# Kernel optimization log

Measured on AMD Instinct MI355X. Metric: run time of the kernel, lower is better.

## Reference

```python
import jax, jax.numpy as jnp
import numpy as np

N_COARSE = 100_000
M_FINE = 4 * N_COARSE
GRID = 128
C_IN, C_HID, C_OUT = 32, 64, 32
K3 = 27   # 3x3x3 neighborhood
K2 = 8    # 2x2x2 transposed-conv offsets


def setup_inputs() -> dict:
    rng = np.random.default_rng(0)
    # --- sparse coarse grid: N unique voxels in GRID^3 ---
    lin = np.sort(rng.choice(GRID ** 3, size=N_COARSE, replace=False))
    cx, cy, cz = lin // (GRID * GRID), (lin // GRID) % GRID, lin % GRID
    coords = np.stack([cx, cy, cz], 1).astype(np.int64)
    # --- rulebook: neighbor index per voxel per 3^3 offset (sentinel = N) ---
    offs = np.array([(dx, dy, dz) for dx in (-1, 0, 1) for dy in (-1, 0, 1) for dz in (-1, 0, 1)])
    nbr = np.full((N_COARSE, K3), N_COARSE, np.int32)
    for k in range(K3):
        nc = coords + offs[k]
        valid = ((nc >= 0) & (nc < GRID)).all(1)
        nlin = nc[:, 0] * GRID * GRID + nc[:, 1] * GRID + nc[:, 2]
        pos = np.clip(np.searchsorted(lin, nlin), 0, N_COARSE - 1)
        found = valid & (lin[pos] == nlin)
        nbr[found, k] = pos[found].astype(np.int32)
    # --- fine grid: 4 distinct children (of 8) per coarse voxel ---
    child = np.argsort(rng.random((N_COARSE, K2)), axis=1)[:, :4].astype(np.int32)
    parent_idx = np.repeat(np.arange(N_COARSE, dtype=np.int32), 4)
    offset_idx = child.reshape(-1)

    key = jax.random.key(0)
    ks = jax.random.split(key, 16)
    nrm = lambda k, sh, fan: (jax.random.normal(k, sh, jnp.float32) / np.sqrt(fan)).astype(jnp.float32)
    return {
        "feats_in": jax.random.normal(ks[0], (N_COARSE, C_IN), jnp.float32),
        "x_up_feats": jax.random.normal(ks[1], (M_FINE, C_OUT), jnp.float32),
        "nbr_idx": jnp.asarray(nbr),
        "parent_idx": jnp.asarray(parent_idx),
        "offset_idx": jnp.asarray(offset_idx),
        "W_enc1": nrm(ks[2], (K3, C_IN, C_HID), K3 * C_IN),
        "b_enc1": jnp.zeros((C_HID,), jnp.float32),
        "W_enc2": nrm(ks[3], (K3, C_HID, C_HID), K3 * C_HID),
        "b_enc2": jnp.zeros((C_HID,), jnp.float32),
        "W_enc3": nrm(ks[4], (K3, C_HID, C_HID), K3 * C_HID),
        "b_enc3": jnp.zeros((C_HID,), jnp.float32),
        "W_t": nrm(ks[5], (K2, C_HID, C_HID), C_HID),
        "b_t": jnp.zeros((C_HID,), jnp.float32),
        "W_d1": nrm(ks[6], (C_HID, C_HID), C_HID),
        "b_d1": jnp.zeros((C_HID,), jnp.float32),
        "W_d2": nrm(ks[7], (C_HID, C_OUT), C_HID),
        "b_d2": jnp.zeros((C_OUT,), jnp.float32),
    }


def _sparse_conv3(x, nbr, W, b):
    """3x3x3 stride-1 sparse conv: gather neighbors, per-offset matmul, accumulate.
    x: [N,Cin], nbr: [N,27] (sentinel N -> zero feature), W: [27,Cin,Cout]."""
    xp = jnp.concatenate([x, jnp.zeros((1, x.shape[1]), x.dtype)], 0)  # sentinel row
    acc = jnp.broadcast_to(b, (x.shape[0], W.shape[-1]))
    for k in range(W.shape[0]):  # fixed 27-way structural loop
        acc = acc + xp[nbr[:, k]] @ W[k]
    return acc


def _t_conv2(x, parent_idx, offset_idx, W, b):
    """2x2x2 stride-2 transposed sparse conv onto a given fine grid.
    x: [N,C], parent_idx: [M] (sentinel N), offset_idx: [M] in [0,8)."""
    xp = jnp.concatenate([x, jnp.zeros((1, x.shape[1]), x.dtype)], 0)
    g = xp[parent_idx]  # [M,C]
    out = jnp.broadcast_to(b, (g.shape[0], W.shape[-1]))
    for k in range(W.shape[0]):  # fixed 8-way structural loop
        out = out + jnp.where((offset_idx == k)[:, None], g @ W[k], 0.0)
    return out


def reference(feats_in, x_up_feats, nbr_idx, parent_idx, offset_idx,
              W_enc1, b_enc1, W_enc2, b_enc2, W_enc3, b_enc3,
              W_t, b_t, W_d1, b_d1, W_d2, b_d2):
    # encoder: (conv -> dropout[eval: identity] -> relu) x 3
    x = jax.nn.relu(_sparse_conv3(feats_in, nbr_idx, W_enc1, b_enc1))
    x = jax.nn.relu(_sparse_conv3(x, nbr_idx, W_enc2, b_enc2))
    x = jax.nn.relu(_sparse_conv3(x, nbr_idx, W_enc3, b_enc3))
    # transposed upsample conv onto x_upsample's grid
    x = _t_conv2(x, parent_idx, offset_idx, W_t, b_t)
    # decoder: relu -> 1x1 conv -> relu -> 1x1 conv, then residual add
    x = jax.nn.relu(x) @ W_d1 + b_d1
    x = jax.nn.relu(x) @ W_d2 + b_d2
    return x + x_up_feats
```

## Files before the change

### kernel.cpp

```cpp
#include <hip/hip_runtime.h>
#include <hip/hip_bf16.h>

#define NC 100000
#define MF 400000
#define K3 27

typedef __bf16 bf16_t;
typedef bf16_t bf16x8 __attribute__((ext_vector_type(8)));
typedef float  f32x4  __attribute__((ext_vector_type(4)));

#define O_E1 0
#define O_E2 55296
#define O_E3 165888
#define O_T  276480
#define O_D1 309248
#define O_D2 313344
#define W_TOTAL 315392

__device__ __align__(16) bf16_t g_w[W_TOTAL];
__device__ __align__(16) bf16_t g_x0[(size_t)NC * 32];
__device__ __align__(16) bf16_t g_x1[(size_t)NC * 64];
__device__ __align__(16) bf16_t g_x2[(size_t)NC * 64];
__device__ int g_nbrT[(size_t)K3 * NC];

static __device__ __forceinline__ bf16x8 zero8() {
    bf16x8 v;
#pragma unroll
    for (int i = 0; i < 8; ++i) v[i] = (bf16_t)0.0f;
    return v;
}

__global__ __launch_bounds__(256) void prep_k(
    const float* __restrict__ W_e1, const float* __restrict__ W_e2,
    const float* __restrict__ W_e3, const float* __restrict__ W_t,
    const float* __restrict__ W_d1, const float* __restrict__ W_d2,
    const float* __restrict__ feats, const int* __restrict__ nbr)
{
    int b = blockIdx.x;
    if (b < 154) {
        int tid = b * 256 + threadIdx.x;
        int lane = tid & 63;
        int f = tid >> 6;
        const float* src; int doff, nt, nc, fb;
        if      (f < 108) { src = W_e1; doff = O_E1; nt = 4; nc = 1; fb = 0;   }
        else if (f < 324) { src = W_e2; doff = O_E2; nt = 4; nc = 2; fb = 108; }
        else if (f < 540) { src = W_e3; doff = O_E3; nt = 4; nc = 2; fb = 324; }
        else if (f < 604) { src = W_t;  doff = O_T;  nt = 4; nc = 2; fb = 540; }
        else if (f < 612) { src = W_d1; doff = O_D1; nt = 4; nc = 2; fb = 604; }
        else              { src = W_d2; doff = O_D2; nt = 2; nc = 2; fb = 612; }
        int lf = f - fb;
        int t  = lf % nt;
        int c  = (lf / nt) % nc;
        int ko = lf / (nt * nc);
        int Cin = nc * 32, Cout = nt * 16;
        int n  = t * 16 + (lane & 15);
        int kb = c * 32 + (lane >> 4) * 8;
        bf16x8 tmp;
#pragma unroll
        for (int j = 0; j < 8; ++j)
            tmp[j] = (bf16_t)src[((size_t)ko * Cin + (kb + j)) * Cout + n];
        *(bf16x8*)(g_w + doff + (size_t)lf * 512 + lane * 8) = tmp;
    } else if (b < 1717) {
        int i = (b - 154) * 256 + threadIdx.x;
        if (i < NC * 32 / 8) {
            const f32x4* p = (const f32x4*)(feats + (size_t)i * 8);
            f32x4 lo = p[0], hi = p[1];
            bf16x8 v;
#pragma unroll
            for (int j = 0; j < 4; ++j) { v[j] = (bf16_t)lo[j]; v[j + 4] = (bf16_t)hi[j]; }
            *(bf16x8*)(g_x0 + (size_t)i * 8) = v;
        }
    } else {
        int r = (b - 1717) * 256 + threadIdx.x;
        if (r < NC) {
#pragma unroll
            for (int k = 0; k < K3; ++k)
                g_nbrT[(size_t)k * NC + r] = nbr[(size_t)r * K3 + k];
        }
    }
}

#define TS 72
template <int CH>
__global__ __launch_bounds__(128) void conv_k(
    int w_off,
    const float* __restrict__ bias,
    int src_sel, int dst_sel)
{
    constexpr int CIN = CH * 32;
    const bf16_t* xb = (src_sel == 0) ? g_x0 : (src_sel == 1 ? g_x1 : g_x2);
    bf16_t* y = (dst_sel == 1) ? g_x1 : g_x2;
    const bf16_t* wsrc = g_w + w_off;

    __shared__ __align__(16) bf16_t bB[2][4096];
    int tid = threadIdx.x;
    int wv = tid >> 6, lane = tid & 63;
    int cl = lane & 15, q = lane >> 4;

    int per = gridDim.x >> 3;
    int blk = (blockIdx.x & 7) * per + (blockIdx.x >> 3);
    int base = (blk * 2 + wv) * 64;

    {
        const bf16x8* s = (const bf16x8*)wsrc;
        bf16x8* d = (bf16x8*)bB[0];
#pragma unroll
        for (int i = 0; i < CH * 2; ++i) d[i * 128 + tid] = s[i * 128 + tid];
    }
    __syncthreads();

    f32x4 acc[4][4];
#pragma unroll
    for (int t = 0; t < 4; ++t) {
        float b = bias[t * 16 + cl];
#pragma unroll
        for (int mt = 0; mt < 4; ++mt) acc[mt][t] = (f32x4){b, b, b, b};
    }

    for (int ko = 0; ko < K3; ++ko) {
        int cur = ko & 1;
        if (ko + 1 < K3) {
            const bf16x8* s = (const bf16x8*)(wsrc + (size_t)(ko + 1) * CH * 2048);
            bf16x8* d = (bf16x8*)bB[cur ^ 1];
#pragma unroll
            for (int i = 0; i < CH * 2; ++i) d[i * 128 + tid] = s[i * 128 + tid];
        }
        int idx[4];
#pragma unroll
        for (int mt = 0; mt < 4; ++mt) {
            int r = base + mt * 16 + cl;
            idx[mt] = (r < NC) ? g_nbrT[(size_t)ko * NC + r] : NC;
        }
#pragma unroll
        for (int c = 0; c < CH; ++c) {
            bf16x8 bfr[4];
#pragma unroll
            for (int t = 0; t < 4; ++t)
                bfr[t] = *(const bf16x8*)&bB[cur][(c * 4 + t) * 512 + lane * 8];
#pragma unroll
            for (int mt = 0; mt < 4; ++mt) {
                bool valid = (unsigned)idx[mt] < (unsigned)NC;
                int s = valid ? idx[mt] : 0;
                bf16x8 a = *(const bf16x8*)(xb + (size_t)s * CIN + c * 32 + q * 8);
                if (!valid) a = zero8();
#pragma unroll
                for (int t = 0; t < 4; ++t)
                    acc[mt][t] = __builtin_amdgcn_mfma_f32_16x16x32_bf16(
                        a, bfr[t], acc[mt][t], 0, 0, 0);
            }
        }
        __syncthreads();
    }

    bf16_t* tb = ((bf16_t*)bB) + wv * 2304;
#pragma unroll
    for (int ch = 0; ch < 2; ++ch) {
#pragma unroll
        for (int mt2 = 0; mt2 < 2; ++mt2)
#pragma unroll
            for (int t = 0; t < 4; ++t)
#pragma unroll
                for (int r = 0; r < 4; ++r) {
                    float v = acc[ch * 2 + mt2][t][r];
                    v = v > 0.0f ? v : 0.0f;
                    tb[(mt2 * 16 + q * 4 + r) * TS + t * 16 + cl] = (bf16_t)v;
                }
#pragma unroll
        for (int i = 0; i < 4; ++i) {
            int rl = i * 8 + (lane >> 3);
            int c8 = (lane & 7) * 8;
            bf16x8 v8 = *(const bf16x8*)&tb[rl * TS + c8];
            int orow = base + ch * 32 + rl;
            if (orow < NC)
                *(bf16x8*)(y + (size_t)orow * 64 + c8) = v8;
        }
    }
}

#define HS 72
__global__ __launch_bounds__(256) void tconv_dec_k(
    const int*   __restrict__ offs,
    const float* __restrict__ b_t,
    const float* __restrict__ b_d1,
    const float* __restrict__ b_d2,
    const float* __restrict__ x_up,
    float*       __restrict__ out)
{
    __shared__ __align__(16) bf16_t h_lds[4][64 * HS];
    __shared__ __align__(16) int off_lds[4][64];
    int wv = threadIdx.x >> 6, lane = threadIdx.x & 63;
    int cl = lane & 15, q = lane >> 4;
    int per = gridDim.x >> 3;
    int blk = (blockIdx.x & 7) * per + (blockIdx.x >> 3);
    int p0 = (blk * 4 + wv) * 16;
    int fbase = p0 * 4;

    {
        int fi = fbase + lane;
        off_lds[wv][lane] = (fi < MF) ? offs[fi] : 0;
    }
    int code[4];
#pragma unroll
    for (int r = 0; r < 4; ++r) {
        int4 o = *(const int4*)&off_lds[wv][(q * 4 + r) * 4];
        code[r] = (1 << (4 * o.x)) | (2 << (4 * o.y)) |
                  (3 << (4 * o.z)) | (4 << (4 * o.w));
    }

    bool pv = (p0 + cl) < NC;
    size_t xrow = (size_t)(pv ? p0 + cl : 0) * 64;
    bf16x8 ax[2];
#pragma unroll
    for (int c = 0; c < 2; ++c) {
        bf16x8 t8 = *(const bf16x8*)(g_x1 + xrow + c * 32 + q * 8);
        ax[c] = pv ? t8 : zero8();
    }

    const bf16_t* wt = g_w + O_T;
#pragma unroll
    for (int k = 0; k < 8; ++k) {
        f32x4 acc[4];
#pragma unroll
        for (int t = 0; t < 4; ++t) {
            float b = b_t[t * 16 + cl];
            acc[t] = (f32x4){b, b, b, b};
        }
#pragma unroll
        for (int c = 0; c < 2; ++c) {
            const bf16_t* wb = wt + ((size_t)(k * 2 + c) * 4) * 512 + lane * 8;
#pragma unroll
            for (int t = 0; t < 4; ++t) {
                bf16x8 b = *(const bf16x8*)(wb + t * 512);
                acc[t] = __builtin_amdgcn_mfma_f32_16x16x32_bf16(ax[c], b, acc[t], 0, 0, 0);
            }
        }
#pragma unroll
        for (int r = 0; r < 4; ++r) {
            int nib = (code[r] >> (4 * k)) & 0xF;
            if (nib) {
                int fl = (((q * 4 + r) * 4) + (nib - 1)) & 63;
#pragma unroll
                for (int t = 0; t < 4; ++t) {
                    float v = acc[t][r];
                    v = v > 0.0f ? v : 0.0f;
                    h_lds[wv][fl * HS + t * 16 + cl] = (bf16_t)v;
                }
            }
        }
    }

    bf16x8 a1[4][2];
#pragma unroll
    for (int mt = 0; mt < 4; ++mt)
#pragma unroll
        for (int c = 0; c < 2; ++c)
            a1[mt][c] = *(const bf16x8*)&h_lds[wv][(mt * 16 + cl) * HS + c * 32 + q * 8];

#pragma unroll
    for (int mt = 0; mt < 4; ++mt) {
        f32x4 acc2[4];
#pragma unroll
        for (int t = 0; t < 4; ++t) {
            float b = b_d1[t * 16 + cl];
            acc2[t] = (f32x4){b, b, b, b};
        }
#pragma unroll
        for (int c = 0; c < 2; ++c)
#pragma unroll
            for (int t = 0; t < 4; ++t) {
                bf16x8 b = *(const bf16x8*)(g_w + O_D1 + (size_t)(c * 4 + t) * 512 + lane * 8);
                acc2[t] = __builtin_amdgcn_mfma_f32_16x16x32_bf16(a1[mt][c], b, acc2[t], 0, 0, 0);
            }
#pragma unroll
        for (int t = 0; t < 4; ++t)
#pragma unroll
            for (int r = 0; r < 4; ++r) {
                float v = acc2[t][r];
                v = v > 0.0f ? v : 0.0f;
                h_lds[wv][(mt * 16 + q * 4 + r) * HS + t * 16 + cl] = (bf16_t)v;
            }
    }

    float* fW = (float*)h_lds[wv];
#pragma unroll
    for (int mt = 0; mt < 4; ++mt) {
        bf16x8 a2[2];
#pragma unroll
        for (int c = 0; c < 2; ++c)
            a2[c] = *(const bf16x8*)&h_lds[wv][(mt * 16 + cl) * HS + c * 32 + q * 8];
        f32x4 acc3[2];
#pragma unroll
        for (int t = 0; t < 2; ++t) {
            float b = b_d2[t * 16 + cl];
            acc3[t] = (f32x4){b, b, b, b};
        }
#pragma unroll
        for (int c = 0; c < 2; ++c)
#pragma unroll
            for (int t = 0; t < 2; ++t) {
                bf16x8 b = *(const bf16x8*)(g_w + O_D2 + (size_t)(c * 2 + t) * 512 + lane * 8);
                acc3[t] = __builtin_amdgcn_mfma_f32_16x16x32_bf16(a2[c], b, acc3[t], 0, 0, 0);
            }
#pragma unroll
        for (int t = 0; t < 2; ++t)
#pragma unroll
            for (int r = 0; r < 4; ++r)
                fW[(mt * 16 + q * 4 + r) * 36 + t * 16 + cl] = acc3[t][r];
    }

#pragma unroll
    for (int i = 0; i < 8; ++i) {
        int rl = i * 8 + (lane >> 3);
        int c4 = (lane & 7) * 4;
        int fg = fbase + rl;
        if (fg < MF) {
            f32x4 xv = *(const f32x4*)(x_up + (size_t)fg * 32 + c4);
            f32x4 v = *(const f32x4*)&fW[rl * 36 + c4];
            v += xv;
            *(f32x4*)(out + (size_t)fg * 32 + c4) = v;
        }
    }
}

extern "C" void kernel_launch(void* const* d_in, const int* in_sizes, int n_in,
                              void* d_out, int out_size, void* d_ws, size_t ws_size,
                              hipStream_t stream) {
    const float* feats  = (const float*)d_in[0];
    const float* x_up   = (const float*)d_in[1];
    const int*   nbr    = (const int*)d_in[2];
    const int*   offs   = (const int*)d_in[4];
    const float* W_e1 = (const float*)d_in[5];
    const float* b_e1 = (const float*)d_in[6];
    const float* W_e2 = (const float*)d_in[7];
    const float* b_e2 = (const float*)d_in[8];
    const float* W_e3 = (const float*)d_in[9];
    const float* b_e3 = (const float*)d_in[10];
    const float* W_t  = (const float*)d_in[11];
    const float* b_t  = (const float*)d_in[12];
    const float* W_d1 = (const float*)d_in[13];
    const float* b_d1 = (const float*)d_in[14];
    const float* W_d2 = (const float*)d_in[15];
    const float* b_d2 = (const float*)d_in[16];
    float* out = (float*)d_out;

    prep_k<<<2108, 256, 0, stream>>>(W_e1, W_e2, W_e3, W_t, W_d1, W_d2, feats, nbr);

    conv_k<1><<<784, 128, 0, stream>>>(O_E1, b_e1, 0, 1);
    conv_k<2><<<784, 128, 0, stream>>>(O_E2, b_e2, 1, 2);
    conv_k<2><<<784, 128, 0, stream>>>(O_E3, b_e3, 2, 1);

    tconv_dec_k<<<1568, 256, 0, stream>>>(offs, b_t, b_d1, b_d2, x_up, out);
}
```

Baseline: 339.2 us.

## Share conv weight tiles across four waves and prefetch neighbor indices and residuals

Conv blocks grow to four waves so each staged weight tile in LDS serves twice as many rows, halving global weight traffic per row. Neighbor indices for the next kernel offset are loaded during the current step to hide gather latency, and the output transpose gets its own LDS buffer. The decoder kernel stages its 1x1 weights in LDS and issues the residual loads up front. This costs more LDS and registers per block, which may reduce occupancy, and halves the block count.

New measurement: 371.5 us. 9.5% more time.

```diff
diff --git a/kernel.cpp b/kernel.cpp
--- a/kernel.cpp
+++ b/kernel.cpp
@@ -82,7 +82,7 @@
 
 #define TS 72
 template <int CH>
-__global__ __launch_bounds__(128) void conv_k(
+__global__ __launch_bounds__(256) void conv_k(
     int w_off,
     const float* __restrict__ bias,
     int src_sel, int dst_sel)
@@ -93,21 +93,27 @@
     const bf16_t* wsrc = g_w + w_off;
 
     __shared__ __align__(16) bf16_t bB[2][4096];
+    __shared__ __align__(16) bf16_t tbuf[4][2304];
     int tid = threadIdx.x;
     int wv = tid >> 6, lane = tid & 63;
     int cl = lane & 15, q = lane >> 4;
 
     int per = gridDim.x >> 3;
     int blk = (blockIdx.x & 7) * per + (blockIdx.x >> 3);
-    int base = (blk * 2 + wv) * 64;
+    int base = blk * 256 + wv * 64;
 
     {
         const bf16x8* s = (const bf16x8*)wsrc;
         bf16x8* d = (bf16x8*)bB[0];
 #pragma unroll
-        for (int i = 0; i < CH * 2; ++i) d[i * 128 + tid] = s[i * 128 + tid];
-    }
-    __syncthreads();
+        for (int i = 0; i < CH; ++i) d[i * 256 + tid] = s[i * 256 + tid];
+    }
+    int idx[4], idx_n[4];
+#pragma unroll
+    for (int mt = 0; mt < 4; ++mt) {
+        int r = base + mt * 16 + cl;
+        idx[mt] = (r < NC) ? g_nbrT[r] : NC;
+    }
 
     f32x4 acc[4][4];
 #pragma unroll
@@ -116,6 +122,7 @@
 #pragma unroll
         for (int mt = 0; mt < 4; ++mt) acc[mt][t] = (f32x4){b, b, b, b};
     }
+    __syncthreads();
 
     for (int ko = 0; ko < K3; ++ko) {
         int cur = ko & 1;
@@ -123,13 +130,12 @@
             const bf16x8* s = (const bf16x8*)(wsrc + (size_t)(ko + 1) * CH * 2048);
             bf16x8* d = (bf16x8*)bB[cur ^ 1];
 #pragma unroll
-            for (int i = 0; i < CH * 2; ++i) d[i * 128 + tid] = s[i * 128 + tid];
-        }
-        int idx[4];
-#pragma unroll
-        for (int mt = 0; mt < 4; ++mt) {
-            int r = base + mt * 16 + cl;
-            idx[mt] = (r < NC) ? g_nbrT[(size_t)ko * NC + r] : NC;
+            for (int i = 0; i < CH; ++i) d[i * 256 + tid] = s[i * 256 + tid];
+#pragma unroll
+            for (int mt = 0; mt < 4; ++mt) {
+                int r = base + mt * 16 + cl;
+                idx_n[mt] = (r < NC) ? g_nbrT[(size_t)(ko + 1) * NC + r] : NC;
+            }
         }
 #pragma unroll
         for (int c = 0; c < CH; ++c) {
@@ -150,9 +156,11 @@
             }
         }
         __syncthreads();
-    }
-
-    bf16_t* tb = ((bf16_t*)bB) + wv * 2304;
+#pragma unroll
+        for (int mt = 0; mt < 4; ++mt) idx[mt] = idx_n[mt];
+    }
+
+    bf16_t* tb = tbuf[wv];
 #pragma unroll
     for (int ch = 0; ch < 2; ++ch) {
 #pragma unroll
@@ -187,6 +195,7 @@
     float*       __restrict__ out)
 {
     __shared__ __align__(16) bf16_t h_lds[4][64 * HS];
+    __shared__ __align__(16) bf16_t dW[6144];
     __shared__ __align__(16) int off_lds[4][64];
     int wv = threadIdx.x >> 6, lane = threadIdx.x & 63;
     int cl = lane & 15, q = lane >> 4;
@@ -195,10 +204,28 @@
     int p0 = (blk * 4 + wv) * 16;
     int fbase = p0 * 4;
 
+    f32x4 xu[8];
+#pragma unroll
+    for (int i = 0; i < 8; ++i) {
+        int rl = i * 8 + (lane >> 3);
+        int c4 = (lane & 7) * 4;
+        int fg = fbase + rl;
+        if (fg < MF) xu[i] = *(const f32x4*)(x_up + (size_t)fg * 32 + c4);
+        else xu[i] = (f32x4){0.0f, 0.0f, 0.0f, 0.0f};
+    }
+
+    {
+        const bf16x8* s = (const bf16x8*)(g_w + O_D1);
+        bf16x8* d = (bf16x8*)dW;
+#pragma unroll
+        for (int i = 0; i < 3; ++i) d[i * 256 + threadIdx.x] = s[i * 256 + threadIdx.x];
+    }
     {
         int fi = fbase + lane;
         off_lds[wv][lane] = (fi < MF) ? offs[fi] : 0;
     }
+    __syncthreads();
+
     int code[4];
 #pragma unroll
     for (int r = 0; r < 4; ++r) {
@@ -268,7 +295,7 @@
         for (int c = 0; c < 2; ++c)
 #pragma unroll
             for (int t = 0; t < 4; ++t) {
-                bf16x8 b = *(const bf16x8*)(g_w + O_D1 + (size_t)(c * 4 + t) * 512 + lane * 8);
+                bf16x8 b = *(const bf16x8*)&dW[(size_t)(c * 4 + t) * 512 + lane * 8];
                 acc2[t] = __builtin_amdgcn_mfma_f32_16x16x32_bf16(a1[mt][c], b, acc2[t], 0, 0, 0);
             }
 #pragma unroll
@@ -298,7 +325,7 @@
         for (int c = 0; c < 2; ++c)
 #pragma unroll
             for (int t = 0; t < 2; ++t) {
-                bf16x8 b = *(const bf16x8*)(g_w + O_D2 + (size_t)(c * 2 + t) * 512 + lane * 8);
+                bf16x8 b = *(const bf16x8*)&dW[4096 + (size_t)(c * 2 + t) * 512 + lane * 8];
                 acc3[t] = __builtin_amdgcn_mfma_f32_16x16x32_bf16(a2[c], b, acc3[t], 0, 0, 0);
             }
 #pragma unroll
@@ -314,9 +341,8 @@
         int c4 = (lane & 7) * 4;
         int fg = fbase + rl;
         if (fg < MF) {
-            f32x4 xv = *(const f32x4*)(x_up + (size_t)fg * 32 + c4);
             f32x4 v = *(const f32x4*)&fW[rl * 36 + c4];
-            v += xv;
+            v += xu[i];
             *(f32x4*)(out + (size_t)fg * 32 + c4) = v;
         }
     }
@@ -345,9 +371,9 @@
 
     prep_k<<<2108, 256, 0, stream>>>(W_e1, W_e2, W_e3, W_t, W_d1, W_d2, feats, nbr);
 
-    conv_k<1><<<784, 128, 0, stream>>>(O_E1, b_e1, 0, 1);
-    conv_k<2><<<784, 128, 0, stream>>>(O_E2, b_e2, 1, 2);
-    conv_k<2><<<784, 128, 0, stream>>>(O_E3, b_e3, 2, 1);
+    conv_k<1><<<392, 256, 0, stream>>>(O_E1, b_e1, 0, 1);
+    conv_k<2><<<392, 256, 0, stream>>>(O_E2, b_e2, 1, 2);
+    conv_k<2><<<392, 256, 0, stream>>>(O_E3, b_e3, 2, 1);
 
     tconv_dec_k<<<1568, 256, 0, stream>>>(offs, b_t, b_d1, b_d2, x_up, out);
 }
```
